# Kernel tuning notes

Measured on AMD Instinct MI355X. Metric: run time of the kernel, lower is better.

The kernel has to match this reference:

```python
import jax, jax.numpy as jnp
import numpy as np

P, G = 8192, 4096
SH_DEG = 2            # active_sh_degree = max_sh_degree = 2 -> 9 SH coeffs
N_SH = (SH_DEG + 1) ** 2
C0 = 0.28209479177387814
C1 = 0.4886025119029199
C2 = (1.0925484305920792, -1.0925484305920792, 0.31539156525252005,
      -1.0925484305920792, 0.5462742152960396)
CMIN, CMAX = 0.0, 1.0  # config.rendering.coord_min/max


def setup_inputs() -> dict:
    key = jax.random.key(0)
    ks = jax.random.split(key, 7)
    position_rx = jax.random.uniform(ks[0], (P, 3), dtype=jnp.float32)  # in [cmin,cmax]
    mean = jax.random.uniform(ks[1], (G, 3), dtype=jnp.float32) * 2.0 - 1.0
    features_dc = jax.random.uniform(ks[2], (G, 1, 1), dtype=jnp.float32) * 0.2 - 0.1
    features_rest = jax.random.normal(ks[3], (G, 1, N_SH - 1), dtype=jnp.float32) * 0.05
    scaling = jnp.float32(np.log(0.3)) + 0.1 * jax.random.normal(ks[4], (G, 3), dtype=jnp.float32)
    rotation = jax.random.normal(ks[5], (G, 4), dtype=jnp.float32)
    opacity = jax.random.normal(ks[6], (G, 1), dtype=jnp.float32)
    return dict(position_rx=position_rx, mean=mean, features_dc=features_dc,
                features_rest=features_rest, scaling=scaling, rotation=rotation,
                opacity=opacity)


def _quat_to_rot(q):
    # q: [G,4] (w,x,y,z), normalized (rotation_activation = F.normalize)
    q = q / jnp.linalg.norm(q, axis=-1, keepdims=True)
    r, x, y, z = q[:, 0], q[:, 1], q[:, 2], q[:, 3]
    R = jnp.stack([
        jnp.stack([1 - 2 * (y * y + z * z), 2 * (x * y - r * z), 2 * (x * z + r * y)], -1),
        jnp.stack([2 * (x * y + r * z), 1 - 2 * (x * x + z * z), 2 * (y * z - r * x)], -1),
        jnp.stack([2 * (x * z - r * y), 2 * (y * z + r * x), 1 - 2 * (x * x + y * y)], -1),
    ], axis=-2)  # [G,3,3]
    return R


def _eval_sh(sh, dirs):
    # sh: [G, 9]; dirs: [P, G, 3] unit vectors -> [P, G]
    x, y, z = dirs[..., 0], dirs[..., 1], dirs[..., 2]
    res = C0 * sh[:, 0]
    res = (res - C1 * y * sh[:, 1] + C1 * z * sh[:, 2] - C1 * x * sh[:, 3])
    xx, yy, zz = x * x, y * y, z * z
    res = (res
           + C2[0] * (x * y) * sh[:, 4]
           + C2[1] * (y * z) * sh[:, 5]
           + C2[2] * (2.0 * zz - xx - yy) * sh[:, 6]
           + C2[3] * (x * z) * sh[:, 7]
           + C2[4] * (xx - yy) * sh[:, 8])
    return res


def reference(position_rx, mean, features_dc, features_rest, scaling, rotation, opacity):
    # normalize_points: map [cmin,cmax] -> [-1,1]
    q = (position_rx - CMIN) / (CMAX - CMIN) * 2.0 - 1.0  # [P,3]

    # covariance_activation: Sigma = L L^T, L = R diag(s); use precision directly
    scales = jnp.exp(scaling)                    # [G,3]
    inv_var = 1.0 / (scales * scales)            # [G,3]
    R = _quat_to_rot(rotation)                   # [G,3,3]
    Sinv = jnp.einsum('gik,gk,gjk->gij', R, inv_var, R)  # Sigma^{-1} [G,3,3]

    diff = q[:, None, :] - mean[None, :, :]      # [P,G,3]
    mahal = jnp.einsum('pgi,gij,pgj->pg', diff, Sinv, diff)  # [P,G]
    gauss = jnp.exp(-0.5 * mahal)                # [P,G]

    # eval_features: normalized direction point -> gaussian, SH evaluation
    dirs = diff / (jnp.linalg.norm(diff, axis=-1, keepdims=True) + 1e-8)
    sh = jnp.concatenate([features_dc, features_rest], axis=-1)[:, 0, :]  # [G,9]
    feat = _eval_sh(sh, dirs)                    # [P,G]

    alpha = jax.nn.sigmoid(opacity)[:, 0]        # [G]
    out = jnp.einsum('pg,g->p', feat * gauss, alpha)  # splat accumulate
    return out[:, None]                          # [P,1]
```

## Files before the change

### kernel.cpp

```cpp
#include <hip/hip_runtime.h>
#include <hip/hip_bf16.h>

constexpr int P = 8192;
constexpr int G = 4096;
constexpr int BLK = 256;
constexpr int GSPLIT = 128;
constexpr int CHUNK = G / GSPLIT;
constexpr int PPT = 4;
constexpr int PBLK = BLK * PPT;
constexpr float LOG2E = 1.4426950408889634f;

typedef float v2f __attribute__((ext_vector_type(2)));

__device__ __forceinline__ float fast_exp2(float x) {
  float r;
  asm("v_exp_f32 %0, %1" : "=v"(r) : "v"(x));
  return r;
}

__global__ __launch_bounds__(BLK) void fused_main(
    const float* __restrict__ pos,
    const float* __restrict__ mean, const float* __restrict__ fdc,
    const float* __restrict__ frest, const float* __restrict__ scal,
    const float* __restrict__ rot, const float* __restrict__ opac,
    float* __restrict__ partial) {
  __shared__ float4 sg[CHUNK * 5];

  const int t = threadIdx.x;
  const int c = blockIdx.y;
  const int pbase = blockIdx.x * PBLK + t;

  v2f pxv[2], pyv[2], pzv[2], accv[2];
#pragma unroll
  for (int h = 0; h < 2; ++h) {
    const int pA = pbase + (2 * h + 0) * BLK;
    const int pB = pbase + (2 * h + 1) * BLK;
    v2f x = {pos[pA * 3 + 0], pos[pB * 3 + 0]};
    v2f y = {pos[pA * 3 + 1], pos[pB * 3 + 1]};
    v2f z = {pos[pA * 3 + 2], pos[pB * 3 + 2]};
    pxv[h] = x * 2.0f - 1.0f;
    pyv[h] = y * 2.0f - 1.0f;
    pzv[h] = z * 2.0f - 1.0f;
    accv[h] = (v2f){0.f, 0.f};
  }

  if (t < CHUNK) {
    const int g = c * CHUNK + t;

    float qr = rot[g * 4 + 0], qx = rot[g * 4 + 1];
    float qy = rot[g * 4 + 2], qz = rot[g * 4 + 3];
    float qn = 1.0f / sqrtf(qr * qr + qx * qx + qy * qy + qz * qz);
    qr *= qn; qx *= qn; qy *= qn; qz *= qn;

    float R00 = 1.f - 2.f * (qy * qy + qz * qz);
    float R01 = 2.f * (qx * qy - qr * qz);
    float R02 = 2.f * (qx * qz + qr * qy);
    float R10 = 2.f * (qx * qy + qr * qz);
    float R11 = 1.f - 2.f * (qx * qx + qz * qz);
    float R12 = 2.f * (qy * qz - qr * qx);
    float R20 = 2.f * (qx * qz - qr * qy);
    float R21 = 2.f * (qy * qz + qr * qx);
    float R22 = 1.f - 2.f * (qx * qx + qy * qy);

    float sc0 = expf(scal[g * 3 + 0]);
    float sc1 = expf(scal[g * 3 + 1]);
    float sc2 = expf(scal[g * 3 + 2]);
    float iv0 = 1.0f / (sc0 * sc0);
    float iv1 = 1.0f / (sc1 * sc1);
    float iv2 = 1.0f / (sc2 * sc2);

    float s00 = R00 * R00 * iv0 + R01 * R01 * iv1 + R02 * R02 * iv2;
    float s11 = R10 * R10 * iv0 + R11 * R11 * iv1 + R12 * R12 * iv2;
    float s22 = R20 * R20 * iv0 + R21 * R21 * iv1 + R22 * R22 * iv2;
    float s01 = R00 * R10 * iv0 + R01 * R11 * iv1 + R02 * R12 * iv2;
    float s02 = R00 * R20 * iv0 + R01 * R21 * iv1 + R02 * R22 * iv2;
    float s12 = R10 * R20 * iv0 + R11 * R21 * iv1 + R12 * R22 * iv2;

    const float kD = -0.5f * LOG2E;
    const float kO = -LOG2E;

    float alpha = 1.0f / (1.0f + expf(-opac[g]));

    const float C0 = 0.28209479177387814f;
    const float C1 = 0.4886025119029199f;
    float a0 = C0 * fdc[g] * alpha;
    float a1 = -C1 * frest[g * 8 + 0] * alpha;
    float a2 =  C1 * frest[g * 8 + 1] * alpha;
    float a3 = -C1 * frest[g * 8 + 2] * alpha;
    float a4 =  1.0925484305920792f  * frest[g * 8 + 3] * alpha;
    float a5 = -1.0925484305920792f  * frest[g * 8 + 4] * alpha;
    float a6 =  0.31539156525252005f * frest[g * 8 + 5] * alpha;
    float a7 = -1.0925484305920792f  * frest[g * 8 + 6] * alpha;
    float a8 =  0.5462742152960396f  * frest[g * 8 + 7] * alpha;

    float mx = mean[g * 3 + 0], my = mean[g * 3 + 1], mz = mean[g * 3 + 2];

    sg[t * 5 + 0] = make_float4(mx, my, mz, kD * s00);
    sg[t * 5 + 1] = make_float4(kD * s11, kD * s22, kO * s01, kO * s02);
    sg[t * 5 + 2] = make_float4(kO * s12, a0, a1, a2);
    sg[t * 5 + 3] = make_float4(a3, a4, a5, a7);
    sg[t * 5 + 4] = make_float4(a8 - a6, -a8 - a6, 2.f * a6, 0.f);
  }

  __syncthreads();

#pragma unroll 2
  for (int gi = 0; gi < CHUNK; ++gi) {
    const float4 v0 = sg[gi * 5 + 0];
    const float4 v1 = sg[gi * 5 + 1];
    const float4 v2 = sg[gi * 5 + 2];
    const float4 v3 = sg[gi * 5 + 3];
    const float4 v4 = sg[gi * 5 + 4];

#pragma unroll
    for (int h = 0; h < 2; ++h) {
      const v2f dx = pxv[h] - v0.x;
      const v2f dy = pyv[h] - v0.y;
      const v2f dz = pzv[h] - v0.z;
      const v2f dxx = dx * dx, dyy = dy * dy, dzz = dz * dz;
      const v2f dxdy = dx * dy, dxdz = dx * dz, dydz = dy * dz;
      const v2f d2 = dxx + dyy + dzz;

      v2f m = v0.w * dxx;
      m = v1.x * dyy + m;
      m = v1.y * dzz + m;
      m = v1.z * dxdy + m;
      m = v1.w * dxdz + m;
      m = v2.x * dydz + m;
      v2f gauss;
      gauss.x = fast_exp2(m.x);
      gauss.y = fast_exp2(m.y);

      const v2f d2c = __builtin_elementwise_max(d2, (v2f){1e-16f, 1e-16f});
      v2f inv;
      inv.x = __builtin_amdgcn_rsqf(d2c.x);
      inv.y = __builtin_amdgcn_rsqf(d2c.y);
      const v2f inv2 = inv * inv;

      v2f lin = v2.z * dy;
      lin = v2.w * dz + lin;
      lin = v3.x * dx + lin;

      v2f quad = v3.y * dxdy;
      quad = v3.z * dydz + quad;
      quad = v3.w * dxdz + quad;
      quad = v4.x * dxx + quad;
      quad = v4.y * dyy + quad;
      quad = v4.z * dzz + quad;

      v2f feat = inv * lin + v2.y;
      feat = inv2 * quad + feat;

      accv[h] = gauss * feat + accv[h];
    }
  }

#pragma unroll
  for (int h = 0; h < 2; ++h) {
    partial[(size_t)c * P + pbase + (2 * h + 0) * BLK] = accv[h].x;
    partial[(size_t)c * P + pbase + (2 * h + 1) * BLK] = accv[h].y;
  }
}

__global__ __launch_bounds__(256) void reduce_kernel(
    const float* __restrict__ partial, float* __restrict__ out) {
  __shared__ float red[4][64];
  const int t = threadIdx.x;
  const int lane = t & 63;
  const int s = t >> 6;
  const int p = blockIdx.x * 64 + lane;
  const int cbase = s * 32;

  float a0 = 0.f, a1 = 0.f, a2 = 0.f, a3 = 0.f;
#pragma unroll
  for (int j = 0; j < 32; j += 4) {
    a0 += partial[(size_t)(cbase + j + 0) * P + p];
    a1 += partial[(size_t)(cbase + j + 1) * P + p];
    a2 += partial[(size_t)(cbase + j + 2) * P + p];
    a3 += partial[(size_t)(cbase + j + 3) * P + p];
  }
  red[s][lane] = (a0 + a1) + (a2 + a3);
  __syncthreads();

  if (t < 64) {
    out[p] = (red[0][lane] + red[1][lane]) + (red[2][lane] + red[3][lane]);
  }
}

extern "C" void kernel_launch(void* const* d_in, const int* in_sizes, int n_in,
                              void* d_out, int out_size, void* d_ws, size_t ws_size,
                              hipStream_t stream) {
  const float* pos   = (const float*)d_in[0];
  const float* mean  = (const float*)d_in[1];
  const float* fdc   = (const float*)d_in[2];
  const float* frest = (const float*)d_in[3];
  const float* scal  = (const float*)d_in[4];
  const float* rot   = (const float*)d_in[5];
  const float* opac  = (const float*)d_in[6];
  float* out = (float*)d_out;

  float* partial = (float*)d_ws;

  fused_main<<<dim3(P / PBLK, GSPLIT), BLK, 0, stream>>>(
      pos, mean, fdc, frest, scal, rot, opac, partial);
  reduce_kernel<<<P / 64, 256, 0, stream>>>(partial, out);
}
```

Baseline: 30.90 us.

## Hold Gaussian coefficients in registers and cross-lane reduce over points

Per-Gaussian precomputation moves into a separate kernel that writes a structure-of-arrays buffer. The main kernel now maps lanes to Gaussians (4 per lane, coefficients kept in registers) and loops over points, reducing each point's sum across the wavefront with shuffles. The G split drops to 16 chunks, which shrinks the partial buffer and the reduce work. This removes the LDS broadcast reads and the redundant precompute per block, but adds a 6-step shuffle reduction per pair of points, scalar position loads, a third launch, and about 76 live coefficient registers.

```diff
diff --git a/kernel.cpp b/kernel.cpp
--- a/kernel.cpp
+++ b/kernel.cpp
@@ -3,12 +3,14 @@
 
 constexpr int P = 8192;
 constexpr int G = 4096;
-constexpr int BLK = 256;
-constexpr int GSPLIT = 128;
-constexpr int CHUNK = G / GSPLIT;
-constexpr int PPT = 4;
-constexpr int PBLK = BLK * PPT;
 constexpr float LOG2E = 1.4426950408889634f;
+
+constexpr int NCH = 16;
+constexpr int GPC = G / NCH;
+constexpr int NG = 4;
+constexpr int PR = 256;
+constexpr int PPW = P / PR;
+constexpr int NCOEF = 19;
 
 typedef float v2f __attribute__((ext_vector_type(2)));
 
@@ -18,148 +20,177 @@
   return r;
 }
 
-__global__ __launch_bounds__(BLK) void fused_main(
-    const float* __restrict__ pos,
+__global__ __launch_bounds__(256) void precomp_kernel(
     const float* __restrict__ mean, const float* __restrict__ fdc,
     const float* __restrict__ frest, const float* __restrict__ scal,
     const float* __restrict__ rot, const float* __restrict__ opac,
+    float* __restrict__ soa) {
+  int g = blockIdx.x * blockDim.x + threadIdx.x;
+  if (g >= G) return;
+
+  float qr = rot[g * 4 + 0], qx = rot[g * 4 + 1];
+  float qy = rot[g * 4 + 2], qz = rot[g * 4 + 3];
+  float qn = 1.0f / sqrtf(qr * qr + qx * qx + qy * qy + qz * qz);
+  qr *= qn; qx *= qn; qy *= qn; qz *= qn;
+
+  float R00 = 1.f - 2.f * (qy * qy + qz * qz);
+  float R01 = 2.f * (qx * qy - qr * qz);
+  float R02 = 2.f * (qx * qz + qr * qy);
+  float R10 = 2.f * (qx * qy + qr * qz);
+  float R11 = 1.f - 2.f * (qx * qx + qz * qz);
+  float R12 = 2.f * (qy * qz - qr * qx);
+  float R20 = 2.f * (qx * qz - qr * qy);
+  float R21 = 2.f * (qy * qz + qr * qx);
+  float R22 = 1.f - 2.f * (qx * qx + qy * qy);
+
+  float sc0 = expf(scal[g * 3 + 0]);
+  float sc1 = expf(scal[g * 3 + 1]);
+  float sc2 = expf(scal[g * 3 + 2]);
+  float iv0 = 1.0f / (sc0 * sc0);
+  float iv1 = 1.0f / (sc1 * sc1);
+  float iv2 = 1.0f / (sc2 * sc2);
+
+  float s00 = R00 * R00 * iv0 + R01 * R01 * iv1 + R02 * R02 * iv2;
+  float s11 = R10 * R10 * iv0 + R11 * R11 * iv1 + R12 * R12 * iv2;
+  float s22 = R20 * R20 * iv0 + R21 * R21 * iv1 + R22 * R22 * iv2;
+  float s01 = R00 * R10 * iv0 + R01 * R11 * iv1 + R02 * R12 * iv2;
+  float s02 = R00 * R20 * iv0 + R01 * R21 * iv1 + R02 * R22 * iv2;
+  float s12 = R10 * R20 * iv0 + R11 * R21 * iv1 + R12 * R22 * iv2;
+
+  const float kD = -0.5f * LOG2E;
+  const float kO = -LOG2E;
+
+  float alpha = 1.0f / (1.0f + expf(-opac[g]));
+
+  const float C0 = 0.28209479177387814f;
+  const float C1 = 0.4886025119029199f;
+  float a0 = C0 * fdc[g] * alpha;
+  float a1 = -C1 * frest[g * 8 + 0] * alpha;
+  float a2 =  C1 * frest[g * 8 + 1] * alpha;
+  float a3 = -C1 * frest[g * 8 + 2] * alpha;
+  float a4 =  1.0925484305920792f  * frest[g * 8 + 3] * alpha;
+  float a5 = -1.0925484305920792f  * frest[g * 8 + 4] * alpha;
+  float a6 =  0.31539156525252005f * frest[g * 8 + 5] * alpha;
+  float a7 = -1.0925484305920792f  * frest[g * 8 + 6] * alpha;
+  float a8 =  0.5462742152960396f  * frest[g * 8 + 7] * alpha;
+
+  soa[0 * G + g]  = mean[g * 3 + 0];
+  soa[1 * G + g]  = mean[g * 3 + 1];
+  soa[2 * G + g]  = mean[g * 3 + 2];
+  soa[3 * G + g]  = kD * s00;
+  soa[4 * G + g]  = kD * s11;
+  soa[5 * G + g]  = kD * s22;
+  soa[6 * G + g]  = kO * s01;
+  soa[7 * G + g]  = kO * s02;
+  soa[8 * G + g]  = kO * s12;
+  soa[9 * G + g]  = a0;
+  soa[10 * G + g] = a1;
+  soa[11 * G + g] = a2;
+  soa[12 * G + g] = a3;
+  soa[13 * G + g] = a4;
+  soa[14 * G + g] = a5;
+  soa[15 * G + g] = a7;
+  soa[16 * G + g] = a8 - a6;
+  soa[17 * G + g] = -a8 - a6;
+  soa[18 * G + g] = 2.f * a6;
+}
+
+__global__ __launch_bounds__(256) void main_kernel(
+    const float* __restrict__ pos, const float* __restrict__ soa,
     float* __restrict__ partial) {
-  __shared__ float4 sg[CHUNK * 5];
-
   const int t = threadIdx.x;
-  const int c = blockIdx.y;
-  const int pbase = blockIdx.x * PBLK + t;
-
-  v2f pxv[2], pyv[2], pzv[2], accv[2];
-#pragma unroll
-  for (int h = 0; h < 2; ++h) {
-    const int pA = pbase + (2 * h + 0) * BLK;
-    const int pB = pbase + (2 * h + 1) * BLK;
-    v2f x = {pos[pA * 3 + 0], pos[pB * 3 + 0]};
-    v2f y = {pos[pA * 3 + 1], pos[pB * 3 + 1]};
-    v2f z = {pos[pA * 3 + 2], pos[pB * 3 + 2]};
-    pxv[h] = x * 2.0f - 1.0f;
-    pyv[h] = y * 2.0f - 1.0f;
-    pzv[h] = z * 2.0f - 1.0f;
-    accv[h] = (v2f){0.f, 0.f};
-  }
-
-  if (t < CHUNK) {
-    const int g = c * CHUNK + t;
-
-    float qr = rot[g * 4 + 0], qx = rot[g * 4 + 1];
-    float qy = rot[g * 4 + 2], qz = rot[g * 4 + 3];
-    float qn = 1.0f / sqrtf(qr * qr + qx * qx + qy * qy + qz * qz);
-    qr *= qn; qx *= qn; qy *= qn; qz *= qn;
-
-    float R00 = 1.f - 2.f * (qy * qy + qz * qz);
-    float R01 = 2.f * (qx * qy - qr * qz);
-    float R02 = 2.f * (qx * qz + qr * qy);
-    float R10 = 2.f * (qx * qy + qr * qz);
-    float R11 = 1.f - 2.f * (qx * qx + qz * qz);
-    float R12 = 2.f * (qy * qz - qr * qx);
-    float R20 = 2.f * (qx * qz - qr * qy);
-    float R21 = 2.f * (qy * qz + qr * qx);
-    float R22 = 1.f - 2.f * (qx * qx + qy * qy);
-
-    float sc0 = expf(scal[g * 3 + 0]);
-    float sc1 = expf(scal[g * 3 + 1]);
-    float sc2 = expf(scal[g * 3 + 2]);
-    float iv0 = 1.0f / (sc0 * sc0);
-    float iv1 = 1.0f / (sc1 * sc1);
-    float iv2 = 1.0f / (sc2 * sc2);
-
-    float s00 = R00 * R00 * iv0 + R01 * R01 * iv1 + R02 * R02 * iv2;
-    float s11 = R10 * R10 * iv0 + R11 * R11 * iv1 + R12 * R12 * iv2;
-    float s22 = R20 * R20 * iv0 + R21 * R21 * iv1 + R22 * R22 * iv2;
-    float s01 = R00 * R10 * iv0 + R01 * R11 * iv1 + R02 * R12 * iv2;
-    float s02 = R00 * R20 * iv0 + R01 * R21 * iv1 + R02 * R22 * iv2;
-    float s12 = R10 * R20 * iv0 + R11 * R21 * iv1 + R12 * R22 * iv2;
-
-    const float kD = -0.5f * LOG2E;
-    const float kO = -LOG2E;
-
-    float alpha = 1.0f / (1.0f + expf(-opac[g]));
-
-    const float C0 = 0.28209479177387814f;
-    const float C1 = 0.4886025119029199f;
-    float a0 = C0 * fdc[g] * alpha;
-    float a1 = -C1 * frest[g * 8 + 0] * alpha;
-    float a2 =  C1 * frest[g * 8 + 1] * alpha;
-    float a3 = -C1 * frest[g * 8 + 2] * alpha;
-    float a4 =  1.0925484305920792f  * frest[g * 8 + 3] * alpha;
-    float a5 = -1.0925484305920792f  * frest[g * 8 + 4] * alpha;
-    float a6 =  0.31539156525252005f * frest[g * 8 + 5] * alpha;
-    float a7 = -1.0925484305920792f  * frest[g * 8 + 6] * alpha;
-    float a8 =  0.5462742152960396f  * frest[g * 8 + 7] * alpha;
-
-    float mx = mean[g * 3 + 0], my = mean[g * 3 + 1], mz = mean[g * 3 + 2];
-
-    sg[t * 5 + 0] = make_float4(mx, my, mz, kD * s00);
-    sg[t * 5 + 1] = make_float4(kD * s11, kD * s22, kO * s01, kO * s02);
-    sg[t * 5 + 2] = make_float4(kO * s12, a0, a1, a2);
-    sg[t * 5 + 3] = make_float4(a3, a4, a5, a7);
-    sg[t * 5 + 4] = make_float4(a8 - a6, -a8 - a6, 2.f * a6, 0.f);
-  }
-
-  __syncthreads();
-
-#pragma unroll 2
-  for (int gi = 0; gi < CHUNK; ++gi) {
-    const float4 v0 = sg[gi * 5 + 0];
-    const float4 v1 = sg[gi * 5 + 1];
-    const float4 v2 = sg[gi * 5 + 2];
-    const float4 v3 = sg[gi * 5 + 3];
-    const float4 v4 = sg[gi * 5 + 4];
-
-#pragma unroll
-    for (int h = 0; h < 2; ++h) {
-      const v2f dx = pxv[h] - v0.x;
-      const v2f dy = pyv[h] - v0.y;
-      const v2f dz = pzv[h] - v0.z;
-      const v2f dxx = dx * dx, dyy = dy * dy, dzz = dz * dz;
-      const v2f dxdy = dx * dy, dxdz = dx * dz, dydz = dy * dz;
-      const v2f d2 = dxx + dyy + dzz;
-
-      v2f m = v0.w * dxx;
-      m = v1.x * dyy + m;
-      m = v1.y * dzz + m;
-      m = v1.z * dxdy + m;
-      m = v1.w * dxdz + m;
-      m = v2.x * dydz + m;
-      v2f gauss;
-      gauss.x = fast_exp2(m.x);
-      gauss.y = fast_exp2(m.y);
-
-      const v2f d2c = __builtin_elementwise_max(d2, (v2f){1e-16f, 1e-16f});
-      v2f inv;
-      inv.x = __builtin_amdgcn_rsqf(d2c.x);
-      inv.y = __builtin_amdgcn_rsqf(d2c.y);
-      const v2f inv2 = inv * inv;
-
-      v2f lin = v2.z * dy;
-      lin = v2.w * dz + lin;
-      lin = v3.x * dx + lin;
-
-      v2f quad = v3.y * dxdy;
-      quad = v3.z * dydz + quad;
-      quad = v3.w * dxdz + quad;
-      quad = v4.x * dxx + quad;
-      quad = v4.y * dyy + quad;
-      quad = v4.z * dzz + quad;
-
-      v2f feat = inv * lin + v2.y;
-      feat = inv2 * quad + feat;
-
-      accv[h] = gauss * feat + accv[h];
+  const int lane = t & 63;
+  const int w = blockIdx.x * 4 + (t >> 6);
+  const int c = w >> 8;
+  const int r = w & (PR - 1);
+  const int g0 = c * GPC + lane * NG;
+  const int pbase = r * PPW;
+
+  float4 cf[NCOEF];
+#pragma unroll
+  for (int k = 0; k < NCOEF; ++k)
+    cf[k] = *reinterpret_cast<const float4*>(soa + (size_t)k * G + g0);
+
+#define CV(k) (pi == 0 ? (v2f){cf[k].x, cf[k].y} : (v2f){cf[k].z, cf[k].w})
+
+  for (int pass = 0; pass < PPW / 2; ++pass) {
+    const int p0 = pbase + pass * 2;
+
+    float qs0[3], qs1[3];
+    qs0[0] = pos[(p0 + 0) * 3 + 0] * 2.0f - 1.0f;
+    qs0[1] = pos[(p0 + 0) * 3 + 1] * 2.0f - 1.0f;
+    qs0[2] = pos[(p0 + 0) * 3 + 2] * 2.0f - 1.0f;
+    qs1[0] = pos[(p0 + 1) * 3 + 0] * 2.0f - 1.0f;
+    qs1[1] = pos[(p0 + 1) * 3 + 1] * 2.0f - 1.0f;
+    qs1[2] = pos[(p0 + 1) * 3 + 2] * 2.0f - 1.0f;
+
+    v2f acc0 = {0.f, 0.f}, acc1 = {0.f, 0.f};
+
+#pragma unroll
+    for (int j = 0; j < 2; ++j) {
+      const float* qs = (j == 0) ? qs0 : qs1;
+      const v2f qx = {qs[0], qs[0]};
+      const v2f qy = {qs[1], qs[1]};
+      const v2f qz = {qs[2], qs[2]};
+      v2f accl = {0.f, 0.f};
+
+#pragma unroll
+      for (int pi = 0; pi < 2; ++pi) {
+        const v2f dx = qx - CV(0);
+        const v2f dy = qy - CV(1);
+        const v2f dz = qz - CV(2);
+        const v2f dxx = dx * dx, dyy = dy * dy, dzz = dz * dz;
+        const v2f dxdy = dx * dy, dxdz = dx * dz, dydz = dy * dz;
+        const v2f d2 = dxx + dyy + dzz;
+
+        v2f m = CV(3) * dxx;
+        m = CV(4) * dyy + m;
+        m = CV(5) * dzz + m;
+        m = CV(6) * dxdy + m;
+        m = CV(7) * dxdz + m;
+        m = CV(8) * dydz + m;
+        v2f gauss;
+        gauss.x = fast_exp2(m.x);
+        gauss.y = fast_exp2(m.y);
+
+        const v2f d2c = __builtin_elementwise_max(d2, (v2f){1e-16f, 1e-16f});
+        v2f inv;
+        inv.x = __builtin_amdgcn_rsqf(d2c.x);
+        inv.y = __builtin_amdgcn_rsqf(d2c.y);
+        const v2f inv2 = inv * inv;
+
+        v2f lin = CV(10) * dy;
+        lin = CV(11) * dz + lin;
+        lin = CV(12) * dx + lin;
+
+        v2f quad = CV(13) * dxdy;
+        quad = CV(14) * dydz + quad;
+        quad = CV(15) * dxdz + quad;
+        quad = CV(16) * dxx + quad;
+        quad = CV(17) * dyy + quad;
+        quad = CV(18) * dzz + quad;
+
+        v2f feat = inv * lin + CV(9);
+        feat = inv2 * quad + feat;
+
+        accl = gauss * feat + accl;
+      }
+      if (j == 0) acc0 = accl; else acc1 = accl;
+    }
+
+    float s0 = acc0.x + acc0.y;
+    float s1 = acc1.x + acc1.y;
+#pragma unroll
+    for (int md = 1; md < 64; md <<= 1) {
+      s0 += __shfl_xor(s0, md, 64);
+      s1 += __shfl_xor(s1, md, 64);
+    }
+    if (lane == 0) {
+      partial[(size_t)c * P + p0 + 0] = s0;
+      partial[(size_t)c * P + p0 + 1] = s1;
     }
   }
-
-#pragma unroll
-  for (int h = 0; h < 2; ++h) {
-    partial[(size_t)c * P + pbase + (2 * h + 0) * BLK] = accv[h].x;
-    partial[(size_t)c * P + pbase + (2 * h + 1) * BLK] = accv[h].y;
-  }
+#undef CV
 }
 
 __global__ __launch_bounds__(256) void reduce_kernel(
@@ -169,16 +200,12 @@
   const int lane = t & 63;
   const int s = t >> 6;
   const int p = blockIdx.x * 64 + lane;
-  const int cbase = s * 32;
-
-  float a0 = 0.f, a1 = 0.f, a2 = 0.f, a3 = 0.f;
-#pragma unroll
-  for (int j = 0; j < 32; j += 4) {
-    a0 += partial[(size_t)(cbase + j + 0) * P + p];
-    a1 += partial[(size_t)(cbase + j + 1) * P + p];
-    a2 += partial[(size_t)(cbase + j + 2) * P + p];
-    a3 += partial[(size_t)(cbase + j + 3) * P + p];
-  }
+  const int cbase = s * 4;
+
+  float a0 = partial[(size_t)(cbase + 0) * P + p];
+  float a1 = partial[(size_t)(cbase + 1) * P + p];
+  float a2 = partial[(size_t)(cbase + 2) * P + p];
+  float a3 = partial[(size_t)(cbase + 3) * P + p];
   red[s][lane] = (a0 + a1) + (a2 + a3);
   __syncthreads();
 
@@ -199,9 +226,10 @@
   const float* opac  = (const float*)d_in[6];
   float* out = (float*)d_out;
 
-  float* partial = (float*)d_ws;
-
-  fused_main<<<dim3(P / PBLK, GSPLIT), BLK, 0, stream>>>(
-      pos, mean, fdc, frest, scal, rot, opac, partial);
+  float* soa = (float*)d_ws;
+  float* partial = (float*)((char*)d_ws + (size_t)NCOEF * G * sizeof(float));
+
+  precomp_kernel<<<G / 256, 256, 0, stream>>>(mean, fdc, frest, scal, rot, opac, soa);
+  main_kernel<<<NCH * PR / 4, 256, 0, stream>>>(pos, soa, partial);
   reduce_kernel<<<P / 64, 256, 0, stream>>>(partial, out);
 }
```

After: 41.54 us. 1.34x slower.
